# Kernel tuning notes

Hardware: AMD Instinct MI355X
Metric: run time of the kernel (lower is better)

The kernel has to match this reference:

```python
import jax, jax.numpy as jnp
import numpy as np
import math

SIZE = 64
SCALE = math.sqrt(SIZE)
EPS = 1e-12  # torch F.normalize default eps

def l2_normalize(x, axis):
    n = jnp.linalg.norm(x, ord=2, axis=axis, keepdims=True)
    return x / jnp.maximum(n, EPS)

def setup_inputs() -> dict:
    key = jax.random.key(0)
    k1, k2, k3 = jax.random.split(key, 3)
    n, l, s, d, v = 8, 2048, 2048, SIZE, SIZE
    return {
        "query": jax.random.normal(k1, (n, l, d), dtype=jnp.float32),
        "key": jax.random.normal(k2, (n, s, d), dtype=jnp.float32),
        "value": jax.random.normal(k3, (n, s, v), dtype=jnp.float32),
        "mask": jnp.ones((n, l, s), dtype=bool),
    }

def reference(query, key, value, mask):
    # rank-3 query path with normalize=True (cosine attention)
    q = l2_normalize(query, 2)
    k = l2_normalize(key, 2)
    score = jnp.einsum('nlk,nsk->nls', q, k) / SCALE
    score = jnp.where(mask, score, -jnp.inf)
    score = jax.nn.softmax(score, axis=2)  # [n, l, s]
    # equivalent to (score.unsqueeze(3) * value.unsqueeze(1)).sum(2)
    output_value = jnp.einsum('nls,nsv->nlv', score, value)
    return (output_value, score)
```

## Files before the change

### kernel.cpp

```cpp
#include <hip/hip_runtime.h>
#include <hip/hip_bf16.h>
#include <math.h>


typedef __bf16 bf16x8 __attribute__((ext_vector_type(8)));
typedef __bf16 bf16x4 __attribute__((ext_vector_type(4)));
typedef float f32x4 __attribute__((ext_vector_type(4)));

#define NB 8
#define LL 2048
#define SS 2048
#define DD 64

__global__ __launch_bounds__(256) void prep_norm(const float* __restrict__ q,
                                                 const float* __restrict__ k,
                                                 __bf16* __restrict__ Qb,
                                                 __bf16* __restrict__ Kb) {
  int w = threadIdx.x >> 6, lane = threadIdx.x & 63;
  int r = blockIdx.x * 4 + w;
  const float* src;
  __bf16* dst;
  float extra;
  if (r < NB * LL) {
    src = q + (size_t)r * DD;
    dst = Qb + (size_t)r * DD;
    extra = 0.125f;
  } else {
    int rk = r - NB * LL;
    src = k + (size_t)rk * DD;
    dst = Kb + (size_t)rk * DD;
    extra = 1.0f;
  }
  float x = src[lane];
  float ss = x * x;
  ss += __shfl_xor(ss, 1);
  ss += __shfl_xor(ss, 2);
  ss += __shfl_xor(ss, 4);
  ss += __shfl_xor(ss, 8);
  ss += __shfl_xor(ss, 16);
  ss += __shfl_xor(ss, 32);
  float nrm = sqrtf(ss);
  float sc = extra / fmaxf(nrm, 1e-12f);
  dst[lane] = (__bf16)(x * sc);
}

__global__ __launch_bounds__(256) void prep_vt(const float* __restrict__ v,
                                               __bf16* __restrict__ Vt) {
  __shared__ __bf16 tile[64][72];
  int n = blockIdx.y;
  int s0 = blockIdx.x * 64;
  int t = threadIdx.x;
#pragma unroll
  for (int it = 0; it < 4; ++it) {
    int idx = t + it * 256;
    int s = idx >> 4, c = idx & 15;
    float4 f = *(const float4*)(v + ((size_t)(n * SS + s0 + s)) * DD + c * 4);
    tile[s][c * 4 + 0] = (__bf16)f.x;
    tile[s][c * 4 + 1] = (__bf16)f.y;
    tile[s][c * 4 + 2] = (__bf16)f.z;
    tile[s][c * 4 + 3] = (__bf16)f.w;
  }
  __syncthreads();
#pragma unroll
  for (int it = 0; it < 4; ++it) {
    int idx = t + it * 256;
    int vv = idx >> 4, c = idx & 15;
    bf16x4 o;
    o[0] = tile[c * 4 + 0][vv];
    o[1] = tile[c * 4 + 1][vv];
    o[2] = tile[c * 4 + 2][vv];
    o[3] = tile[c * 4 + 3][vv];
    *(bf16x4*)(Vt + ((size_t)(n * DD + vv)) * SS + s0 + c * 4) = o;
  }
}

__global__ __launch_bounds__(256, 4) void attn_main(const __bf16* __restrict__ Qb,
                                                    const __bf16* __restrict__ Kb,
                                                    const __bf16* __restrict__ Vt,
                                                    const int* __restrict__ mask,
                                                    float* __restrict__ out_val,
                                                    float* __restrict__ out_score) {
  __shared__ __bf16 e_lds[2][16][72];
  __shared__ float rs_lds[4][16];

  const int n = blockIdx.y;
  const int l0 = blockIdx.x * 16;
  const int t = threadIdx.x;
  const int w = t >> 6;
  const int lane = t & 63;
  const int m16 = lane & 15;
  const int quad = lane >> 4;

  const __bf16* qrow = Qb + ((size_t)(n * LL + l0 + m16)) * DD;
  bf16x8 aq0 = *(const bf16x8*)(qrow + quad * 8);
  bf16x8 aq1 = *(const bf16x8*)(qrow + 32 + quad * 8);

  const __bf16* kbase = Kb + (size_t)n * SS * DD;
  const __bf16* vbase = Vt + (size_t)n * DD * SS;
  const size_t mrow_base = ((size_t)(n * LL + l0)) * SS;

  f32x4 acc_o = {0.f, 0.f, 0.f, 0.f};
  float rsum[4] = {0.f, 0.f, 0.f, 0.f};

  for (int c = 0; c < SS / 64; ++c) {
    const int sc = c * 64;
    const int scol = sc + w * 16 + m16;
    const __bf16* krow = kbase + (size_t)scol * DD;
    bf16x8 b0 = *(const bf16x8*)(krow + quad * 8);
    bf16x8 b1 = *(const bf16x8*)(krow + 32 + quad * 8);
    f32x4 acc = {0.f, 0.f, 0.f, 0.f};
    acc = __builtin_amdgcn_mfma_f32_16x16x32_bf16(aq0, b0, acc, 0, 0, 0);
    acc = __builtin_amdgcn_mfma_f32_16x16x32_bf16(aq1, b1, acc, 0, 0, 0);
#pragma unroll
    for (int r = 0; r < 4; ++r) {
      int row = quad * 4 + r;
      int mk = mask[mrow_base + (size_t)row * SS + scol];
      float e = mk ? __expf(acc[r]) : 0.0f;
      rsum[r] += e;
      e_lds[c & 1][row][w * 16 + m16] = (__bf16)e;
    }
    __syncthreads();
#pragma unroll
    for (int ks = 0; ks < 2; ++ks) {
      bf16x8 ae = *(const bf16x8*)(&e_lds[c & 1][m16][ks * 32 + quad * 8]);
      bf16x8 bv = *(const bf16x8*)(vbase + (size_t)(16 * w + m16) * SS + sc + ks * 32 + quad * 8);
      acc_o = __builtin_amdgcn_mfma_f32_16x16x32_bf16(ae, bv, acc_o, 0, 0, 0);
    }
  }

#pragma unroll
  for (int r = 0; r < 4; ++r) {
    float s = rsum[r];
    s += __shfl_xor(s, 1);
    s += __shfl_xor(s, 2);
    s += __shfl_xor(s, 4);
    s += __shfl_xor(s, 8);
    rsum[r] = s;
  }
  if (m16 == 0) {
#pragma unroll
    for (int r = 0; r < 4; ++r) rs_lds[w][quad * 4 + r] = rsum[r];
  }
  __syncthreads();
  float inv[4];
#pragma unroll
  for (int r = 0; r < 4; ++r) {
    int row = quad * 4 + r;
    float s = rs_lds[0][row] + rs_lds[1][row] + rs_lds[2][row] + rs_lds[3][row];
    inv[r] = 1.0f / s;
  }

#pragma unroll
  for (int r = 0; r < 4; ++r) {
    int row = quad * 4 + r;
    out_val[((size_t)(n * LL + l0 + row)) * DD + 16 * w + m16] = acc_o[r] * inv[r];
  }

  for (int c = 0; c < SS / 64; ++c) {
    const int sc = c * 64;
    const int scol = sc + w * 16 + m16;
    const __bf16* krow = kbase + (size_t)scol * DD;
    bf16x8 b0 = *(const bf16x8*)(krow + quad * 8);
    bf16x8 b1 = *(const bf16x8*)(krow + 32 + quad * 8);
    f32x4 acc = {0.f, 0.f, 0.f, 0.f};
    acc = __builtin_amdgcn_mfma_f32_16x16x32_bf16(aq0, b0, acc, 0, 0, 0);
    acc = __builtin_amdgcn_mfma_f32_16x16x32_bf16(aq1, b1, acc, 0, 0, 0);
#pragma unroll
    for (int r = 0; r < 4; ++r) {
      int row = quad * 4 + r;
      size_t idx = mrow_base + (size_t)row * SS + scol;
      int mk = mask[idx];
      out_score[idx] = mk ? __expf(acc[r]) * inv[r] : 0.0f;
    }
  }
}

extern "C" void kernel_launch(void* const* d_in, const int* in_sizes, int n_in,
                              void* d_out, int out_size, void* d_ws, size_t ws_size,
                              hipStream_t stream) {
  const float* q = (const float*)d_in[0];
  const float* k = (const float*)d_in[1];
  const float* v = (const float*)d_in[2];
  const int* mask = (const int*)d_in[3];

  float* out_val = (float*)d_out;
  float* out_score = out_val + (size_t)NB * LL * DD;

  __bf16* Qb = (__bf16*)d_ws;
  __bf16* Kb = Qb + (size_t)NB * LL * DD;
  __bf16* Vt = Kb + (size_t)NB * SS * DD;

  prep_norm<<<dim3((NB * LL * 2) / 4), dim3(256), 0, stream>>>(q, k, Qb, Kb);
  prep_vt<<<dim3(SS / 64, NB), dim3(256), 0, stream>>>(v, Vt);
  attn_main<<<dim3(LL / 16, NB), dim3(256), 0, stream>>>(Qb, Kb, Vt, mask, out_val, out_score);
}
```

Measured before the change: 330.4 us.

## Pack mask to bitmask, prefetch K/V tiles, use nontemporal score stores

A new pre-pass kernel turns the int mask into a 64-bit-per-row-segment bitmask using ballot. The attention kernel then stages that bitmask for its 16 rows in LDS, so it no longer reads the full int mask twice from global memory. The K and V fragment loads are software-prefetched one chunk ahead, and the score output is written with nontemporal stores. The cost is one extra kernel launch that reads the mask once, plus extra workspace and LDS.

```diff
diff --git a/kernel.cpp b/kernel.cpp
--- a/kernel.cpp
+++ b/kernel.cpp
@@ -11,6 +11,21 @@
 #define LL 2048
 #define SS 2048
 #define DD 64
+#define WORDS (SS / 32)
+
+__global__ __launch_bounds__(256) void pack_mask(const int* __restrict__ mask,
+                                                 unsigned long long* __restrict__ bm) {
+  const int w = threadIdx.x >> 6, lane = threadIdx.x & 63;
+  const size_t gw = (size_t)blockIdx.x * 4 + w;
+  const size_t stride = (size_t)gridDim.x * 4;
+#pragma unroll
+  for (int i = 0; i < 4; ++i) {
+    size_t seg = gw + (size_t)i * stride;
+    int m = __builtin_nontemporal_load(mask + seg * 64 + lane);
+    unsigned long long b = __ballot(m != 0);
+    if (lane == 0) bm[seg] = b;
+  }
+}
 
 __global__ __launch_bounds__(256) void prep_norm(const float* __restrict__ q,
                                                  const float* __restrict__ k,
@@ -77,11 +92,12 @@
 __global__ __launch_bounds__(256, 4) void attn_main(const __bf16* __restrict__ Qb,
                                                     const __bf16* __restrict__ Kb,
                                                     const __bf16* __restrict__ Vt,
-                                                    const int* __restrict__ mask,
+                                                    const unsigned* __restrict__ bm32,
                                                     float* __restrict__ out_val,
                                                     float* __restrict__ out_score) {
   __shared__ __bf16 e_lds[2][16][72];
   __shared__ float rs_lds[4][16];
+  __shared__ unsigned bm_t[WORDS][16];
 
   const int n = blockIdx.y;
   const int l0 = blockIdx.x * 16;
@@ -91,41 +107,65 @@
   const int m16 = lane & 15;
   const int quad = lane >> 4;
 
+  {
+    int word = t & 63, wv = t >> 6;
+#pragma unroll
+    for (int i = 0; i < 4; ++i) {
+      int row = wv * 4 + i;
+      bm_t[word][row] = bm32[(((size_t)(n * LL + l0 + row)) << 6) + word];
+    }
+  }
+
   const __bf16* qrow = Qb + ((size_t)(n * LL + l0 + m16)) * DD;
   bf16x8 aq0 = *(const bf16x8*)(qrow + quad * 8);
   bf16x8 aq1 = *(const bf16x8*)(qrow + 32 + quad * 8);
 
   const __bf16* kbase = Kb + (size_t)n * SS * DD;
-  const __bf16* vbase = Vt + (size_t)n * DD * SS;
+  const __bf16* vbase = Vt + (size_t)n * DD * SS + (size_t)(16 * w + m16) * SS;
   const size_t mrow_base = ((size_t)(n * LL + l0)) * SS;
+  const int scol_off = w * 16 + m16;
+  const unsigned shift = (unsigned)(scol_off & 31);
+  const int word_off = scol_off >> 5;
 
   f32x4 acc_o = {0.f, 0.f, 0.f, 0.f};
   float rsum[4] = {0.f, 0.f, 0.f, 0.f};
 
+  const __bf16* krow0 = kbase + (size_t)scol_off * DD;
+  bf16x8 kb0 = *(const bf16x8*)(krow0 + quad * 8);
+  bf16x8 kb1 = *(const bf16x8*)(krow0 + 32 + quad * 8);
+  bf16x8 vb0 = *(const bf16x8*)(vbase + quad * 8);
+  bf16x8 vb1 = *(const bf16x8*)(vbase + 32 + quad * 8);
+
+  __syncthreads();
+
   for (int c = 0; c < SS / 64; ++c) {
-    const int sc = c * 64;
-    const int scol = sc + w * 16 + m16;
-    const __bf16* krow = kbase + (size_t)scol * DD;
-    bf16x8 b0 = *(const bf16x8*)(krow + quad * 8);
-    bf16x8 b1 = *(const bf16x8*)(krow + 32 + quad * 8);
+    const int cn = (c + 1) & 31;
+    const __bf16* krow_n = kbase + (size_t)(cn * 64 + scol_off) * DD;
+    bf16x8 nkb0 = *(const bf16x8*)(krow_n + quad * 8);
+    bf16x8 nkb1 = *(const bf16x8*)(krow_n + 32 + quad * 8);
+    bf16x8 nvb0 = *(const bf16x8*)(vbase + cn * 64 + quad * 8);
+    bf16x8 nvb1 = *(const bf16x8*)(vbase + cn * 64 + 32 + quad * 8);
+
     f32x4 acc = {0.f, 0.f, 0.f, 0.f};
-    acc = __builtin_amdgcn_mfma_f32_16x16x32_bf16(aq0, b0, acc, 0, 0, 0);
-    acc = __builtin_amdgcn_mfma_f32_16x16x32_bf16(aq1, b1, acc, 0, 0, 0);
+    acc = __builtin_amdgcn_mfma_f32_16x16x32_bf16(aq0, kb0, acc, 0, 0, 0);
+    acc = __builtin_amdgcn_mfma_f32_16x16x32_bf16(aq1, kb1, acc, 0, 0, 0);
+
+    const uint4 mw = *(const uint4*)&bm_t[c * 2 + word_off][quad * 4];
 #pragma unroll
     for (int r = 0; r < 4; ++r) {
-      int row = quad * 4 + r;
-      int mk = mask[mrow_base + (size_t)row * SS + scol];
+      unsigned mk = ((&mw.x)[r] >> shift) & 1u;
       float e = mk ? __expf(acc[r]) : 0.0f;
       rsum[r] += e;
-      e_lds[c & 1][row][w * 16 + m16] = (__bf16)e;
+      e_lds[c & 1][quad * 4 + r][w * 16 + m16] = (__bf16)e;
     }
     __syncthreads();
-#pragma unroll
-    for (int ks = 0; ks < 2; ++ks) {
-      bf16x8 ae = *(const bf16x8*)(&e_lds[c & 1][m16][ks * 32 + quad * 8]);
-      bf16x8 bv = *(const bf16x8*)(vbase + (size_t)(16 * w + m16) * SS + sc + ks * 32 + quad * 8);
-      acc_o = __builtin_amdgcn_mfma_f32_16x16x32_bf16(ae, bv, acc_o, 0, 0, 0);
-    }
+
+    bf16x8 ae0 = *(const bf16x8*)(&e_lds[c & 1][m16][quad * 8]);
+    bf16x8 ae1 = *(const bf16x8*)(&e_lds[c & 1][m16][32 + quad * 8]);
+    acc_o = __builtin_amdgcn_mfma_f32_16x16x32_bf16(ae0, vb0, acc_o, 0, 0, 0);
+    acc_o = __builtin_amdgcn_mfma_f32_16x16x32_bf16(ae1, vb1, acc_o, 0, 0, 0);
+
+    kb0 = nkb0; kb1 = nkb1; vb0 = nvb0; vb1 = nvb1;
   }
 
 #pragma unroll
@@ -156,22 +196,28 @@
     out_val[((size_t)(n * LL + l0 + row)) * DD + 16 * w + m16] = acc_o[r] * inv[r];
   }
 
+  bf16x8 pk0 = *(const bf16x8*)(krow0 + quad * 8);
+  bf16x8 pk1 = *(const bf16x8*)(krow0 + 32 + quad * 8);
   for (int c = 0; c < SS / 64; ++c) {
-    const int sc = c * 64;
-    const int scol = sc + w * 16 + m16;
-    const __bf16* krow = kbase + (size_t)scol * DD;
-    bf16x8 b0 = *(const bf16x8*)(krow + quad * 8);
-    bf16x8 b1 = *(const bf16x8*)(krow + 32 + quad * 8);
+    const int cn = (c + 1) & 31;
+    const __bf16* krow_n = kbase + (size_t)(cn * 64 + scol_off) * DD;
+    bf16x8 nk0 = *(const bf16x8*)(krow_n + quad * 8);
+    bf16x8 nk1 = *(const bf16x8*)(krow_n + 32 + quad * 8);
+
     f32x4 acc = {0.f, 0.f, 0.f, 0.f};
-    acc = __builtin_amdgcn_mfma_f32_16x16x32_bf16(aq0, b0, acc, 0, 0, 0);
-    acc = __builtin_amdgcn_mfma_f32_16x16x32_bf16(aq1, b1, acc, 0, 0, 0);
+    acc = __builtin_amdgcn_mfma_f32_16x16x32_bf16(aq0, pk0, acc, 0, 0, 0);
+    acc = __builtin_amdgcn_mfma_f32_16x16x32_bf16(aq1, pk1, acc, 0, 0, 0);
+
+    const uint4 mw = *(const uint4*)&bm_t[c * 2 + word_off][quad * 4];
+    const int scol = c * 64 + scol_off;
 #pragma unroll
     for (int r = 0; r < 4; ++r) {
-      int row = quad * 4 + r;
-      size_t idx = mrow_base + (size_t)row * SS + scol;
-      int mk = mask[idx];
-      out_score[idx] = mk ? __expf(acc[r]) * inv[r] : 0.0f;
+      unsigned mk = ((&mw.x)[r] >> shift) & 1u;
+      float val = mk ? __expf(acc[r]) * inv[r] : 0.0f;
+      size_t idx = mrow_base + (size_t)(quad * 4 + r) * SS + scol;
+      __builtin_nontemporal_store(val, out_score + idx);
     }
+    pk0 = nk0; pk1 = nk1;
   }
 }
 
@@ -189,8 +235,11 @@
   __bf16* Qb = (__bf16*)d_ws;
   __bf16* Kb = Qb + (size_t)NB * LL * DD;
   __bf16* Vt = Kb + (size_t)NB * SS * DD;
-
+  unsigned long long* bm = (unsigned long long*)(Vt + (size_t)NB * DD * SS);
+
+  pack_mask<<<dim3(32768), dim3(256), 0, stream>>>(mask, bm);
   prep_norm<<<dim3((NB * LL * 2) / 4), dim3(256), 0, stream>>>(q, k, Qb, Kb);
   prep_vt<<<dim3(SS / 64, NB), dim3(256), 0, stream>>>(v, Vt);
-  attn_main<<<dim3(LL / 16, NB), dim3(256), 0, stream>>>(Qb, Kb, Vt, mask, out_val, out_score);
-}
+  attn_main<<<dim3(LL / 16, NB), dim3(256), 0, stream>>>(Qb, Kb, Vt, (const unsigned*)bm,
+                                                         out_val, out_score);
+}
```

Result: slower. 339.6 us (+2.8%).
